# Kernel optimization log

Hardware: AMD Instinct MI355X
Metric: run time of the kernel (lower is better)

The kernel has to match this reference:

```python
import jax, jax.numpy as jnp
import numpy as np

B, T, U, D = 4, 320, 80, 512  # batch, enc frames, dec steps, per-stream dim
INNER, VOCAB, MAX_RLE = 512, 6, 50


def setup_inputs() -> dict:
    key = jax.random.key(0)
    ks = jax.random.split(key, 8)
    s = 0.02
    return {
        "enc_state": jax.random.normal(ks[0], (B, T, D), dtype=jnp.float32),
        "dec_state": jax.random.normal(ks[1], (B, U, D), dtype=jnp.float32),
        "W_f": jax.random.normal(ks[2], (INNER, 2 * D), dtype=jnp.float32) * s,
        "b_f": jax.random.normal(ks[3], (INNER,), dtype=jnp.float32) * s,
        "W_base": jax.random.normal(ks[4], (VOCAB, INNER), dtype=jnp.float32) * s,
        "b_base": jax.random.normal(ks[5], (VOCAB,), dtype=jnp.float32) * s,
        "W_rle": jax.random.normal(ks[6], (MAX_RLE, INNER), dtype=jnp.float32) * s,
        "b_rle": jax.random.normal(ks[7], (MAX_RLE,), dtype=jnp.float32) * s,
    }


def reference(enc_state, dec_state, W_f, b_f, W_base, b_base, W_rle, b_rle):
    # Tile enc [B,T,1,D] and dec [B,1,U,D] to [B,T,U,D] each, concat on last dim.
    t, u = enc_state.shape[1], dec_state.shape[1]
    enc = jnp.broadcast_to(enc_state[:, :, None, :], (enc_state.shape[0], t, u, enc_state.shape[-1]))
    dec = jnp.broadcast_to(dec_state[:, None, :, :], (dec_state.shape[0], t, u, dec_state.shape[-1]))
    concat = jnp.concatenate([enc, dec], axis=-1)  # [B,T,U,2D]
    h = jnp.tanh(jnp.einsum('btuk,ik->btui', concat, W_f) + b_f)  # [B,T,U,INNER]
    base_out = jnp.einsum('btui,vi->btuv', h, W_base) + b_base  # [B,T,U,VOCAB]
    rle_out = jnp.einsum('btui,ri->btur', h, W_rle) + b_rle      # [B,T,U,MAX_RLE]
    return (base_out, rle_out)
```

## Files before the change

### kernel.cpp

```cpp
#include <hip/hip_runtime.h>

typedef float f32x4 __attribute__((ext_vector_type(4)));
typedef short s16x8 __attribute__((ext_vector_type(8)));
typedef unsigned short u16;
typedef unsigned int u32;


__device__ __forceinline__ u16 f2bf(float f) {
  u32 u = __float_as_uint(f);
  u32 r = (u + 0x7FFFu + ((u >> 16) & 1u)) >> 16;
  return (u16)r;
}

__device__ __forceinline__ u32 cvt_pk_bf16(float lo, float hi) {
  u32 r;
  asm("v_cvt_pk_bf16_f32 %0, %1, %2" : "=v"(r) : "v"(lo), "v"(hi));
  return r;
}

__device__ __forceinline__ s16x8 pack8(f32x4 x0, f32x4 x1) {
  union { s16x8 vv; u32 ww[4]; } o;
  o.ww[0] = cvt_pk_bf16(x0[0], x0[1]);
  o.ww[1] = cvt_pk_bf16(x0[2], x0[3]);
  o.ww[2] = cvt_pk_bf16(x1[0], x1[1]);
  o.ww[3] = cvt_pk_bf16(x1[2], x1[3]);
  return o.vv;
}

__device__ __forceinline__ float fast_tanh(float x) {
  float e = __expf(2.f * x);
  return __builtin_fmaf(-2.f, __builtin_amdgcn_rcpf(e + 1.f), 1.f);
}

__device__ __forceinline__ void async16(const float* g, float* l) {
  __builtin_amdgcn_global_load_lds(
      (const __attribute__((address_space(1))) unsigned int*)g,
      (__attribute__((address_space(3))) unsigned int*)l, 16, 0, 0);
}

__global__ void prep_all(const float* __restrict__ enc, const float* __restrict__ dec,
                         s16x8* __restrict__ Xb,
                         const float* __restrict__ Wf, s16x8* __restrict__ WfF,
                         const float* __restrict__ Wb, const float* __restrict__ bb,
                         const float* __restrict__ Wr, const float* __restrict__ br,
                         u16* __restrict__ WoF, float* __restrict__ bias_cat) {
  int bx = blockIdx.x;
  int tid = threadIdx.x;
  if (bx < 400) {
    int idx = bx * 256 + tid;
    long e = (long)idx * 8;
    const float* src = (e < 655360) ? (enc + e) : (dec + (e - 655360));
    Xb[idx] = pack8(*(const f32x4*)src, *(const f32x4*)(src + 4));
  } else if (bx < 656) {
    int id = (bx - 400) * 256 + tid;
    int lane = id & 63;
    int kk = (id >> 6) & 15;
    int nt = (id >> 10) & 31;
    int part = id >> 15;
    int n = nt * 16 + (lane & 15);
    int k = part * 512 + kk * 32 + ((lane >> 4) << 3);
    const float* p = Wf + (long)n * 1024 + k;
    WfF[id] = pack8(*(const f32x4*)p, *(const f32x4*)(p + 4));
  } else {
    int idx = (bx - 656) * 256 + tid;
    int j = idx & 7;
    int lane = (idx >> 3) & 63;
    int ks = (idx >> 9) & 15;
    int nt = idx >> 13;
    int v = nt * 16 + (lane & 15);
    int k = ks * 32 + ((lane >> 4) << 3) + j;
    float val = (v < 6) ? Wb[v * 512 + k] : (v < 56 ? Wr[(v - 6) * 512 + k] : 0.f);
    WoF[idx] = f2bf(val);
    if (bx == 656 && tid < 64) {
      int vv = tid;
      bias_cat[vv] = (vv < 6) ? bb[vv] : (vv < 56 ? br[vv - 6] : 0.f);
    }
  }
}

__global__ __launch_bounds__(256) void egemm(const s16x8* __restrict__ Xb,
                                             const s16x8* __restrict__ WfF,
                                             const float* __restrict__ b_f,
                                             float* __restrict__ Ebf,
                                             float* __restrict__ Dc) {
  int ms = blockIdx.x >> 3;
  int ns = blockIdx.x & 7;
  int w = threadIdx.x >> 6, l = threadIdx.x & 63;
  int r0 = ms * 64 + w * 16;
  int part = (r0 >= 1280) ? 1 : 0;
  int n0 = ns * 64;
  int lrow = r0 + (l & 15);
  int khi = (l >> 4) << 3;
  f32x4 acc[4] = {};
#pragma unroll
  for (int kk = 0; kk < 16; ++kk) {
    s16x8 a = Xb[lrow * 64 + kk * 4 + (khi >> 3)];
#pragma unroll
    for (int nt = 0; nt < 4; ++nt) {
      int ntg = ns * 4 + nt;
      s16x8 bf = WfF[((part * 32 + ntg) * 16 + kk) * 64 + l];
      acc[nt] = __builtin_amdgcn_mfma_f32_16x16x32_bf16(a, bf, acc[nt], 0, 0, 0);
    }
  }
#pragma unroll
  for (int nt = 0; nt < 4; ++nt) {
    int n = n0 + nt * 16 + (l & 15);
    float bias = part ? 0.f : b_f[n];
#pragma unroll
    for (int q = 0; q < 4; ++q) {
      int row = r0 + ((l >> 4) << 2) + q;
      float val = acc[nt][q] + bias;
      if (part) Dc[(row - 1280) * 512 + n] = val;
      else      Ebf[row * 512 + n] = val;
    }
  }
}

__global__ __launch_bounds__(64, 4) void joint_main(const float* __restrict__ Ebf,
                                                    const float* __restrict__ Dc,
                                                    const s16x8* __restrict__ WoF,
                                                    const float* __restrict__ bias_cat,
                                                    float* __restrict__ out) {
  __shared__ __align__(16) float buf[2][1024];
  int bid = blockIdx.x;
  int pair = bid / 5, uf = bid - pair * 5;
  int bt0 = pair * 2;
  int b = pair / 160;
  int u0 = uf * 16;
  int l = threadIdx.x;
  int row = l & 15, hi = l >> 4;

  const float* DcB = Dc + (long)(b * 80 + u0) * 512;
  const float* Eb  = Ebf + (long)bt0 * 512;

  float bias[4];
#pragma unroll
  for (int nt = 0; nt < 4; ++nt) bias[nt] = bias_cat[nt * 16 + row];
  f32x4 acc[2][4];
#pragma unroll
  for (int tt = 0; tt < 2; ++tt)
#pragma unroll
    for (int nt = 0; nt < 4; ++nt) acc[tt][nt] = f32x4{0.f, 0.f, 0.f, 0.f};

#pragma unroll
  for (int r = 0; r < 4; ++r) {
    int srow = r * 4 + hi;
    async16(DcB + srow * 512 + ((row ^ (srow & 7)) << 2), &buf[0][(r * 64 + l) * 4]);
  }

#pragma unroll
  for (int c = 0; c < 8; ++c) {
    __syncthreads();
    __builtin_amdgcn_sched_barrier(0);
    if (c < 7) {
#pragma unroll
      for (int r = 0; r < 4; ++r) {
        int srow = r * 4 + hi;
        async16(DcB + srow * 512 + (c + 1) * 64 + ((row ^ (srow & 7)) << 2),
                &buf[(c + 1) & 1][(r * 64 + l) * 4]);
      }
    }
    s16x8 bfr[8];
#pragma unroll
    for (int kk = 0; kk < 2; ++kk)
#pragma unroll
      for (int nt = 0; nt < 4; ++nt)
        bfr[kk * 4 + nt] = WoF[(nt * 16 + c * 2 + kk) * 64 + l];

    const float* buf_c = buf[c & 1];
#pragma unroll
    for (int kk = 0; kk < 2; ++kk) {
      int g0 = kk * 8 + hi * 2;
      f32x4 dA = *(const f32x4*)(buf_c + row * 64 + ((g0 ^ (row & 7)) << 2));
      f32x4 dB = *(const f32x4*)(buf_c + row * 64 + (((g0 + 1) ^ (row & 7)) << 2));
#pragma unroll
      for (int tt = 0; tt < 2; ++tt) {
        const float* ep = Eb + tt * 512 + c * 64 + kk * 32 + hi * 8;
        f32x4 eA = *(const f32x4*)ep;
        f32x4 eB = *(const f32x4*)(ep + 4);
        float t[8];
#pragma unroll
        for (int j = 0; j < 4; ++j) {
          t[j]     = fast_tanh(eA[j] + dA[j]);
          t[j + 4] = fast_tanh(eB[j] + dB[j]);
        }
        union { s16x8 vv; u32 ww[4]; } ha;
#pragma unroll
        for (int k = 0; k < 4; ++k) ha.ww[k] = cvt_pk_bf16(t[2 * k], t[2 * k + 1]);
        s16x8 afr = ha.vv;
#pragma unroll
        for (int nt = 0; nt < 4; ++nt)
          acc[tt][nt] = __builtin_amdgcn_mfma_f32_16x16x32_bf16(afr, bfr[kk * 4 + nt],
                                                               acc[tt][nt], 0, 0, 0);
      }
    }
  }

#pragma unroll
  for (int tt = 0; tt < 2; ++tt) {
#pragma unroll
    for (int nt = 0; nt < 4; ++nt) {
      int v = nt * 16 + row;
#pragma unroll
      for (int q = 0; q < 4; ++q) {
        long p = (long)(bt0 + tt) * 80 + u0 + hi * 4 + q;
        float val = acc[tt][nt][q] + bias[nt];
        if (v < 6)       out[p * 6 + v] = val;
        else if (v < 56) out[614400 + p * 50 + (v - 6)] = val;
      }
    }
  }
}

extern "C" void kernel_launch(void* const* d_in, const int* in_sizes, int n_in,
                              void* d_out, int out_size, void* d_ws, size_t ws_size,
                              hipStream_t stream) {
  (void)in_sizes; (void)n_in; (void)out_size; (void)ws_size;
  const float* enc = (const float*)d_in[0];
  const float* dec = (const float*)d_in[1];
  const float* Wf  = (const float*)d_in[2];
  const float* bf  = (const float*)d_in[3];
  const float* Wb  = (const float*)d_in[4];
  const float* bb  = (const float*)d_in[5];
  const float* Wr  = (const float*)d_in[6];
  const float* br  = (const float*)d_in[7];
  float* out = (float*)d_out;
  char* ws = (char*)d_ws;

  s16x8* Xb     = (s16x8*)(ws);
  s16x8* WfF    = (s16x8*)(ws + 1638400);
  u16*   WoF    = (u16*)(ws + 2686976);
  float* biasC  = (float*)(ws + 2752512);
  float* Ebf    = (float*)(ws + 2752768);
  float* Dc     = (float*)(ws + 5374208);

  prep_all<<<784, 256, 0, stream>>>(enc, dec, Xb, Wf, WfF, Wb, bb, Wr, br, WoF, biasC);
  egemm<<<200, 256, 0, stream>>>(Xb, WfF, bf, Ebf, Dc);
  joint_main<<<3200, 64, 0, stream>>>(Ebf, Dc, (const s16x8*)WoF, biasC, out);
}
```

Before: 51.40 us.

## Split joint K dimension across four waves and shrink egemm tiles

The joint kernel goes from one wave per block to four waves, each handling a quarter of the 512-wide inner dimension. Each wave prefetches its own Dc slice into shared memory up front instead of running an 8-step double-buffered pipeline. Partial accumulators are then reduced through shared memory, and each wave writes one 16-column output tile. The egemm kernel uses one 16x16 tile per wave and four times as many blocks, which raises parallelism. The costs are the cross-wave reduction, a larger shared-memory footprint (32KB per block), and redundant recomputation-free but more block overhead.

```diff
diff --git a/kernel.cpp b/kernel.cpp
--- a/kernel.cpp
+++ b/kernel.cpp
@@ -86,56 +86,49 @@
   int ms = blockIdx.x >> 3;
   int ns = blockIdx.x & 7;
   int w = threadIdx.x >> 6, l = threadIdx.x & 63;
-  int r0 = ms * 64 + w * 16;
+  int r0 = ms * 16;
   int part = (r0 >= 1280) ? 1 : 0;
-  int n0 = ns * 64;
   int lrow = r0 + (l & 15);
-  int khi = (l >> 4) << 3;
-  f32x4 acc[4] = {};
+  int khi3 = l >> 4;
+  int ntg = ns * 4 + w;
+  f32x4 acc = {};
 #pragma unroll
   for (int kk = 0; kk < 16; ++kk) {
-    s16x8 a = Xb[lrow * 64 + kk * 4 + (khi >> 3)];
-#pragma unroll
-    for (int nt = 0; nt < 4; ++nt) {
-      int ntg = ns * 4 + nt;
-      s16x8 bf = WfF[((part * 32 + ntg) * 16 + kk) * 64 + l];
-      acc[nt] = __builtin_amdgcn_mfma_f32_16x16x32_bf16(a, bf, acc[nt], 0, 0, 0);
-    }
-  }
-#pragma unroll
-  for (int nt = 0; nt < 4; ++nt) {
-    int n = n0 + nt * 16 + (l & 15);
-    float bias = part ? 0.f : b_f[n];
-#pragma unroll
-    for (int q = 0; q < 4; ++q) {
-      int row = r0 + ((l >> 4) << 2) + q;
-      float val = acc[nt][q] + bias;
-      if (part) Dc[(row - 1280) * 512 + n] = val;
-      else      Ebf[row * 512 + n] = val;
-    }
-  }
-}
-
-__global__ __launch_bounds__(64, 4) void joint_main(const float* __restrict__ Ebf,
-                                                    const float* __restrict__ Dc,
-                                                    const s16x8* __restrict__ WoF,
-                                                    const float* __restrict__ bias_cat,
-                                                    float* __restrict__ out) {
-  __shared__ __align__(16) float buf[2][1024];
+    s16x8 a = Xb[lrow * 64 + kk * 4 + khi3];
+    s16x8 bf = WfF[((part * 32 + ntg) * 16 + kk) * 64 + l];
+    acc = __builtin_amdgcn_mfma_f32_16x16x32_bf16(a, bf, acc, 0, 0, 0);
+  }
+  int n = ntg * 16 + (l & 15);
+  float bias = part ? 0.f : b_f[n];
+#pragma unroll
+  for (int q = 0; q < 4; ++q) {
+    int row = r0 + ((l >> 4) << 2) + q;
+    float val = acc[q] + bias;
+    if (part) Dc[(row - 1280) * 512 + n] = val;
+    else      Ebf[row * 512 + n] = val;
+  }
+}
+
+__global__ __launch_bounds__(256) void joint_main(const float* __restrict__ Ebf,
+                                                  const float* __restrict__ Dc,
+                                                  const s16x8* __restrict__ WoF,
+                                                  const float* __restrict__ bias_cat,
+                                                  float* __restrict__ out) {
+  __shared__ __align__(16) float dcbuf[4][2][1024];
   int bid = blockIdx.x;
   int pair = bid / 5, uf = bid - pair * 5;
   int bt0 = pair * 2;
   int b = pair / 160;
   int u0 = uf * 16;
-  int l = threadIdx.x;
+  int tid = threadIdx.x;
+  int w = tid >> 6, l = tid & 63;
   int row = l & 15, hi = l >> 4;
+  int koff = w * 128;
 
   const float* DcB = Dc + (long)(b * 80 + u0) * 512;
   const float* Eb  = Ebf + (long)bt0 * 512;
-
-  float bias[4];
-#pragma unroll
-  for (int nt = 0; nt < 4; ++nt) bias[nt] = bias_cat[nt * 16 + row];
+  float bias_v = bias_cat[w * 16 + row];
+
   f32x4 acc[2][4];
 #pragma unroll
   for (int tt = 0; tt < 2; ++tt)
@@ -143,39 +136,39 @@
     for (int nt = 0; nt < 4; ++nt) acc[tt][nt] = f32x4{0.f, 0.f, 0.f, 0.f};
 
 #pragma unroll
-  for (int r = 0; r < 4; ++r) {
-    int srow = r * 4 + hi;
-    async16(DcB + srow * 512 + ((row ^ (srow & 7)) << 2), &buf[0][(r * 64 + l) * 4]);
-  }
-
-#pragma unroll
-  for (int c = 0; c < 8; ++c) {
-    __syncthreads();
-    __builtin_amdgcn_sched_barrier(0);
-    if (c < 7) {
-#pragma unroll
-      for (int r = 0; r < 4; ++r) {
-        int srow = r * 4 + hi;
-        async16(DcB + srow * 512 + (c + 1) * 64 + ((row ^ (srow & 7)) << 2),
-                &buf[(c + 1) & 1][(r * 64 + l) * 4]);
-      }
+  for (int c = 0; c < 2; ++c)
+#pragma unroll
+    for (int r = 0; r < 4; ++r) {
+      int srow = r * 4 + hi;
+      async16(DcB + srow * 512 + koff + c * 64 + ((row ^ (srow & 7)) << 2),
+              &dcbuf[w][c][(r * 64 + l) * 4]);
+    }
+  __builtin_amdgcn_sched_barrier(0);
+  asm volatile("s_waitcnt vmcnt(4)" ::: "memory");
+  __builtin_amdgcn_sched_barrier(0);
+
+#pragma unroll
+  for (int c = 0; c < 2; ++c) {
+    if (c == 1) {
+      asm volatile("s_waitcnt vmcnt(0)" ::: "memory");
+      __builtin_amdgcn_sched_barrier(0);
     }
     s16x8 bfr[8];
 #pragma unroll
     for (int kk = 0; kk < 2; ++kk)
 #pragma unroll
       for (int nt = 0; nt < 4; ++nt)
-        bfr[kk * 4 + nt] = WoF[(nt * 16 + c * 2 + kk) * 64 + l];
-
-    const float* buf_c = buf[c & 1];
+        bfr[kk * 4 + nt] = WoF[(nt * 16 + w * 4 + c * 2 + kk) * 64 + l];
+
+    const float* bc = &dcbuf[w][c][0];
 #pragma unroll
     for (int kk = 0; kk < 2; ++kk) {
       int g0 = kk * 8 + hi * 2;
-      f32x4 dA = *(const f32x4*)(buf_c + row * 64 + ((g0 ^ (row & 7)) << 2));
-      f32x4 dB = *(const f32x4*)(buf_c + row * 64 + (((g0 + 1) ^ (row & 7)) << 2));
+      f32x4 dA = *(const f32x4*)(bc + row * 64 + ((g0 ^ (row & 7)) << 2));
+      f32x4 dB = *(const f32x4*)(bc + row * 64 + (((g0 + 1) ^ (row & 7)) << 2));
 #pragma unroll
       for (int tt = 0; tt < 2; ++tt) {
-        const float* ep = Eb + tt * 512 + c * 64 + kk * 32 + hi * 8;
+        const float* ep = Eb + tt * 512 + koff + c * 64 + kk * 32 + hi * 8;
         f32x4 eA = *(const f32x4*)ep;
         f32x4 eB = *(const f32x4*)(ep + 4);
         float t[8];
@@ -191,23 +184,35 @@
 #pragma unroll
         for (int nt = 0; nt < 4; ++nt)
           acc[tt][nt] = __builtin_amdgcn_mfma_f32_16x16x32_bf16(afr, bfr[kk * 4 + nt],
-                                                               acc[tt][nt], 0, 0, 0);
+                                                                acc[tt][nt], 0, 0, 0);
       }
     }
   }
 
+  float* red = &dcbuf[0][0][0];
+  asm volatile("s_waitcnt lgkmcnt(0)" ::: "memory");
+  __builtin_amdgcn_sched_barrier(0);
+#pragma unroll
+  for (int tt = 0; tt < 2; ++tt)
+#pragma unroll
+    for (int nt = 0; nt < 4; ++nt)
+      *(f32x4*)(red + ((w * 8 + tt * 4 + nt) * 256 + l * 4)) = acc[tt][nt];
+  __syncthreads();
+
 #pragma unroll
   for (int tt = 0; tt < 2; ++tt) {
-#pragma unroll
-    for (int nt = 0; nt < 4; ++nt) {
-      int v = nt * 16 + row;
-#pragma unroll
-      for (int q = 0; q < 4; ++q) {
-        long p = (long)(bt0 + tt) * 80 + u0 + hi * 4 + q;
-        float val = acc[tt][nt][q] + bias[nt];
-        if (v < 6)       out[p * 6 + v] = val;
-        else if (v < 56) out[614400 + p * 50 + (v - 6)] = val;
-      }
+    f32x4 s = f32x4{0.f, 0.f, 0.f, 0.f};
+#pragma unroll
+    for (int ww = 0; ww < 4; ++ww)
+      s += *(const f32x4*)(red + ((ww * 8 + tt * 4 + w) * 256 + l * 4));
+    long pbase = (long)(bt0 + tt) * 80 + u0;
+    int v = w * 16 + row;
+#pragma unroll
+    for (int q = 0; q < 4; ++q) {
+      long p = pbase + hi * 4 + q;
+      float val = s[q] + bias_v;
+      if (v < 6)       out[p * 6 + v] = val;
+      else if (v < 56) out[614400 + p * 50 + (v - 6)] = val;
     }
   }
 }
@@ -235,6 +240,6 @@
   float* Dc     = (float*)(ws + 5374208);
 
   prep_all<<<784, 256, 0, stream>>>(enc, dec, Xb, Wf, WfF, Wb, bb, Wr, br, WoF, biasC);
-  egemm<<<200, 256, 0, stream>>>(Xb, WfF, bf, Ebf, Dc);
-  joint_main<<<3200, 64, 0, stream>>>(Ebf, Dc, (const s16x8*)WoF, biasC, out);
-}
+  egemm<<<800, 256, 0, stream>>>(Xb, WfF, bf, Ebf, Dc);
+  joint_main<<<3200, 256, 0, stream>>>(Ebf, Dc, (const s16x8*)WoF, biasC, out);
+}
```

New measurement: 48.93 us. 1.05x faster.
